# Performance work log

Hardware: AMD Instinct MI355X
Metric: run time of the kernel (lower is better)

The kernel has to match this reference:

```python
import jax, jax.numpy as jnp
import numpy as np
import math

B, T, C, H, L, V = 8, 511, 1024, 16, 8, 128  # T = block_size - 1
D = C // H
FF = 4 * C


def setup_inputs() -> dict:
    key = jax.random.key(0)
    ks = jax.random.split(key, 12)
    std = 0.02
    n = lambda k, s: (jax.random.normal(k, s, dtype=jnp.float32) * std)
    idx = jax.random.randint(ks[0], (B, T), 0, V)
    idx = jnp.where(idx == 2, 3, idx)  # avoid pad token so logits[idx!=2] keeps all rows
    return {
        "idx": idx,
        "tok_emb": n(ks[1], (V, C)),
        "pos_emb": n(ks[2], (T, C)),
        "ln1_w": jnp.ones((L, C)), "ln1_b": jnp.zeros((L, C)),
        "Wq": n(ks[3], (L, C, C)), "bq": jnp.zeros((L, C)),
        "Wk": n(ks[4], (L, C, C)), "bk": jnp.zeros((L, C)),
        "Wv": n(ks[5], (L, C, C)), "bv": jnp.zeros((L, C)),
        "Wp": n(ks[6], (L, C, C)), "bp": jnp.zeros((L, C)),
        "ln2_w": jnp.ones((L, C)), "ln2_b": jnp.zeros((L, C)),
        "W1": n(ks[7], (L, C, FF)), "b1": jnp.zeros((L, FF)),
        "W2": n(ks[8], (L, FF, C)), "b2": jnp.zeros((L, C)),
        "lnf_w": jnp.ones((C,)), "lnf_b": jnp.zeros((C,)),
        "head_w": n(ks[9], (V, C)),
    }


def _ln(x, w, b):
    m = x.mean(-1, keepdims=True)
    v = ((x - m) ** 2).mean(-1, keepdims=True)
    return (x - m) * jax.lax.rsqrt(v + 1e-5) * w + b


def reference(idx, tok_emb, pos_emb, ln1_w, ln1_b, Wq, bq, Wk, bk, Wv, bv, Wp, bp,
              ln2_w, ln2_b, W1, b1, W2, b2, lnf_w, lnf_b, head_w):
    x = tok_emb[idx] + pos_emb[None, :, :]                      # [B,T,C]
    mask = jnp.tril(jnp.ones((T, T), dtype=bool))
    scale = 1.0 / math.sqrt(D)

    def block(x, p):
        h = _ln(x, p["ln1_w"], p["ln1_b"])
        q = (h @ p["Wq"] + p["bq"]).reshape(B, T, H, D).transpose(0, 2, 1, 3)
        k = (h @ p["Wk"] + p["bk"]).reshape(B, T, H, D).transpose(0, 2, 1, 3)
        v = (h @ p["Wv"] + p["bv"]).reshape(B, T, H, D).transpose(0, 2, 1, 3)
        att = jnp.einsum('bhqd,bhkd->bhqk', q, k) * scale       # [B,H,T,T]
        att = jnp.where(mask, att, -jnp.inf)
        att = jax.nn.softmax(att, axis=-1)
        y = jnp.einsum('bhqk,bhkd->bhqd', att, v)
        y = y.transpose(0, 2, 1, 3).reshape(B, T, C)
        x = x + y @ p["Wp"] + p["bp"]
        h = _ln(x, p["ln2_w"], p["ln2_b"])
        h = jax.nn.gelu(h @ p["W1"] + p["b1"], approximate=False)
        x = x + h @ p["W2"] + p["b2"]
        return x, None

    stacked = dict(ln1_w=ln1_w, ln1_b=ln1_b, Wq=Wq, bq=bq, Wk=Wk, bk=bk, Wv=Wv, bv=bv,
                   Wp=Wp, bp=bp, ln2_w=ln2_w, ln2_b=ln2_b, W1=W1, b1=b1, W2=W2, b2=b2)
    x, _ = jax.lax.scan(block, x, stacked)
    x = _ln(x, lnf_w, lnf_b)
    logits = x @ head_w.T                                       # [B,T,V]
    # logits[idx != 2] with no 2-tokens present == all rows flattened
    return logits.reshape(B * T, V)
```

## Files before the change

kernel.cpp:

```cpp
#include <hip/hip_runtime.h>
#include <hip/hip_bf16.h>

typedef unsigned short u16;
typedef unsigned int   u32;
typedef __attribute__((ext_vector_type(8))) __bf16 bf16x8;
typedef __attribute__((ext_vector_type(4))) float  f32x4;

static constexpr int NB  = 8;
static constexpr int TT  = 511;
static constexpr int CC  = 1024;
static constexpr int HH  = 16;
static constexpr int LL  = 8;
static constexpr int VV  = 128;
static constexpr int FF_ = 4096;
static constexpr int MV  = NB * TT;
static constexpr int MP  = 4096;
static constexpr int TP  = 512;

#define DEVI static __device__ __forceinline__

DEVI u16 f2bf(float f) {
  u32 u = __builtin_bit_cast(u32, f);
  u = (u + 0x7fffu + ((u >> 16) & 1u)) >> 16;
  return (u16)u;
}

DEVI void gload16(const void* g, void* lds) {
  auto gp = (const __attribute__((address_space(1))) u32*)(uintptr_t)g;
  auto lp = (__attribute__((address_space(3))) u32*)(uintptr_t)lds;
  __builtin_amdgcn_global_load_lds(gp, lp, 16, 0, 0);
}

__global__ __launch_bounds__(256) void k_transpose(const float* __restrict__ in,
                                                   u16* __restrict__ out, int K, int N,
                                                   size_t is, size_t os) {
  in  += (size_t)blockIdx.z * is;
  out += (size_t)blockIdx.z * os;
  __shared__ u16 tile[64][66];
  int nb = blockIdx.x * 64, kb = blockIdx.y * 64;
  int t = threadIdx.x;
  int r = t >> 4, c4 = (t & 15) * 4;
#pragma unroll
  for (int i = 0; i < 4; ++i) {
    int k = r + i * 16;
    float4 v = *(const float4*)(in + (size_t)(kb + k) * N + nb + c4);
    tile[k][c4 + 0] = f2bf(v.x); tile[k][c4 + 1] = f2bf(v.y);
    tile[k][c4 + 2] = f2bf(v.z); tile[k][c4 + 3] = f2bf(v.w);
  }
  __syncthreads();
#pragma unroll
  for (int i = 0; i < 4; ++i) {
    int n = r + i * 16;
    ushort4 o;
    o.x = tile[c4 + 0][n]; o.y = tile[c4 + 1][n];
    o.z = tile[c4 + 2][n]; o.w = tile[c4 + 3][n];
    *(ushort4*)(out + (size_t)(nb + n) * K + kb + c4) = o;
  }
}

__global__ __launch_bounds__(256) void k_transpose4(const float* __restrict__ Wq,
                                                    const float* __restrict__ Wk,
                                                    const float* __restrict__ Wv,
                                                    const float* __restrict__ Wp,
                                                    u16* __restrict__ wqkv_t,
                                                    u16* __restrict__ wp_t) {
  int z = blockIdx.z, which = z >> 3, lyr = z & 7;
  const float* in; u16* out;
  size_t sq = (size_t)CC * CC;
  if (which == 0)      { in = Wq + lyr * sq; out = wqkv_t + lyr * 3 * sq; }
  else if (which == 1) { in = Wk + lyr * sq; out = wqkv_t + lyr * 3 * sq + sq; }
  else if (which == 2) { in = Wv + lyr * sq; out = wqkv_t + lyr * 3 * sq + 2 * sq; }
  else                 { in = Wp + lyr * sq; out = wp_t + lyr * sq; }
  __shared__ u16 tile[64][66];
  int nb = blockIdx.x * 64, kb = blockIdx.y * 64;
  int t = threadIdx.x;
  int r = t >> 4, c4 = (t & 15) * 4;
#pragma unroll
  for (int i = 0; i < 4; ++i) {
    int k = r + i * 16;
    float4 v = *(const float4*)(in + (size_t)(kb + k) * CC + nb + c4);
    tile[k][c4 + 0] = f2bf(v.x); tile[k][c4 + 1] = f2bf(v.y);
    tile[k][c4 + 2] = f2bf(v.z); tile[k][c4 + 3] = f2bf(v.w);
  }
  __syncthreads();
#pragma unroll
  for (int i = 0; i < 4; ++i) {
    int n = r + i * 16;
    ushort4 o;
    o.x = tile[c4 + 0][n]; o.y = tile[c4 + 1][n];
    o.z = tile[c4 + 2][n]; o.w = tile[c4 + 3][n];
    *(ushort4*)(out + (size_t)(nb + n) * CC + kb + c4) = o;
  }
}

__global__ __launch_bounds__(256) void k_prep(const float* __restrict__ headw,
                                              const float* __restrict__ bq,
                                              const float* __restrict__ bk,
                                              const float* __restrict__ bv,
                                              u16* __restrict__ headb,
                                              float* __restrict__ bqkv) {
  int i = blockIdx.x * 256 + threadIdx.x;
  if (i < VV * CC) {
    headb[i] = f2bf(headw[i]);
  } else {
    int j = i - VV * CC;
    if (j < LL * 3 * CC) {
      int l = j / (3 * CC), c = j % (3 * CC);
      float v = (c < CC) ? bq[l * CC + c] : (c < 2 * CC) ? bk[l * CC + c - CC] : bv[l * CC + c - 2 * CC];
      bqkv[j] = v;
    }
  }
}

__global__ __launch_bounds__(256) void k_embed(const int* __restrict__ idx,
                                               const float* __restrict__ tok,
                                               const float* __restrict__ pos,
                                               float* __restrict__ x) {
  int row = blockIdx.x;
  int c4 = threadIdx.x * 4;
  if (row >= MV) {
    *(float4*)(x + (size_t)row * CC + c4) = make_float4(0.f, 0.f, 0.f, 0.f);
    return;
  }
  int t = row % TT;
  int tid = idx[row];
  float4 a = *(const float4*)(tok + (size_t)tid * CC + c4);
  float4 p = *(const float4*)(pos + (size_t)t * CC + c4);
  a.x += p.x; a.y += p.y; a.z += p.z; a.w += p.w;
  *(float4*)(x + (size_t)row * CC + c4) = a;
}

__global__ __launch_bounds__(256) void k_ln(const float* __restrict__ x,
                                            const float* __restrict__ w,
                                            const float* __restrict__ b,
                                            u16* __restrict__ out) {
  int wid = threadIdx.x >> 6, l = threadIdx.x & 63;
  int row = blockIdx.x * 4 + wid;
  const float* xr = x + (size_t)row * CC;
  float4 v[4];
  float s = 0.f, sq = 0.f;
#pragma unroll
  for (int i = 0; i < 4; ++i) {
    v[i] = *(const float4*)(xr + (i * 64 + l) * 4);
    s  += v[i].x + v[i].y + v[i].z + v[i].w;
    sq += v[i].x * v[i].x + v[i].y * v[i].y + v[i].z * v[i].z + v[i].w * v[i].w;
  }
#pragma unroll
  for (int o = 32; o; o >>= 1) { s += __shfl_xor(s, o); sq += __shfl_xor(sq, o); }
  float mean = s * (1.f / CC);
  float var  = sq * (1.f / CC) - mean * mean;
  float rs = rsqrtf(var + 1e-5f);
#pragma unroll
  for (int i = 0; i < 4; ++i) {
    int c = (i * 64 + l) * 4;
    float4 wv = *(const float4*)(w + c);
    float4 bv = *(const float4*)(b + c);
    ushort4 o4;
    o4.x = f2bf((v[i].x - mean) * rs * wv.x + bv.x);
    o4.y = f2bf((v[i].y - mean) * rs * wv.y + bv.y);
    o4.z = f2bf((v[i].z - mean) * rs * wv.z + bv.z);
    o4.w = f2bf((v[i].w - mean) * rs * wv.w + bv.w);
    *(ushort4*)(out + (size_t)row * CC + c) = o4;
  }
}

template <int EPI>
__global__ __launch_bounds__(512, 1) void k_gemm4(const u16* __restrict__ A,
                                                  const u16* __restrict__ Wt,
                                                  const float* __restrict__ bias,
                                                  u16* __restrict__ outb,
                                                  u16* __restrict__ vt,
                                                  int N, int K, int gridN) {
  __shared__ char lds[2][4][16384];
  int t = threadIdx.x, l = t & 63, wid = t >> 6;
  int wr = wid >> 2, wc = wid & 3;
  int lr = l & 15, lk16 = (l >> 4) * 16;

  int nwg = gridDim.x, wg = blockIdx.x;
  int qq = nwg >> 3, r8 = nwg & 7;
  int xcd = wg & 7, loc = wg >> 3;
  int swz = (xcd < r8 ? xcd * (qq + 1) : r8 * (qq + 1) + (xcd - r8) * qq) + loc;
  int mblk = swz / gridN, nblk = swz - mblk * gridN;
  int mb = mblk * 256, nb = nblk * 256;
  int NT = K >> 6;
  const u16* Ab = A  + (size_t)mb * K;
  const u16* Bb = Wt + (size_t)nb * K;

  int srow = t >> 3, skb = (t & 7) * 16;

  auto stageH = [&](int kt, int ht) {
    int b = kt & 1;
    const u16* src = (ht < 2) ? Ab : Bb;
    int rowbase = (ht & 1) << 7;
    char* dst = &lds[b][ht][0];
    const u16* s0 = src + (size_t)rowbase * K + kt * 64;
#pragma unroll
    for (int j = 0; j < 2; ++j) {
      int row = j * 64 + srow;
      int kb = skb ^ ((row & 7) << 4);
      gload16(s0 + (size_t)row * K + (kb >> 1), dst + j * 8192 + t * 16);
    }
  };

  f32x4 acc[8][4] = {};

  stageH(0, 0); stageH(0, 1); stageH(0, 2); stageH(0, 3);
  stageH(1, 2); stageH(1, 0); stageH(1, 3);
  asm volatile("s_waitcnt vmcnt(6)" ::: "memory");
  __builtin_amdgcn_s_barrier();
  __builtin_amdgcn_sched_barrier(0);

  for (int kt = 0; kt < NT; kt += 2) {
    bool s2 = (kt + 2) < NT, s3 = (kt + 3) < NT;
#pragma unroll
    for (int half = 0; half < 2; ++half) {
      int buf = half;
      bf16x8 Bf[2][4];
#pragma unroll
      for (int q = 0; q < 4; ++q) {
        bf16x8 Af[2][2];
        if (q == 0) {
#pragma unroll
          for (int ks = 0; ks < 2; ++ks)
#pragma unroll
            for (int nf = 0; nf < 4; ++nf) {
              int grow = ((wc & 1) << 6) + nf * 16 + lr;
              int kb = (ks * 64 + lk16) ^ ((grow & 7) << 4);
              Bf[ks][nf] = *(const bf16x8*)(&lds[buf][2 + (wc >> 1)][0] + grow * 128 + kb);
            }
        }
#pragma unroll
        for (int ks = 0; ks < 2; ++ks)
#pragma unroll
          for (int dm = 0; dm < 2; ++dm) {
            int mf = q * 2 + dm;
            int grow = wr * 64 + (mf & 3) * 16 + lr;
            int kb = (ks * 64 + lk16) ^ ((grow & 7) << 4);
            Af[ks][dm] = *(const bf16x8*)(&lds[buf][mf >> 2][0] + grow * 128 + kb);
          }
        if (half == 0) {
          if (q == 0)      stageH(kt + 1, 1);
          else if (q == 1) { if (s2) stageH(kt + 2, 2); }
          else if (q == 2) { if (s2) stageH(kt + 2, 0); }
          else             { if (s2) stageH(kt + 2, 3); }
        } else {
          if (q == 0)      { if (s2) stageH(kt + 2, 1); }
          else if (q == 1) { if (s3) stageH(kt + 3, 2); }
          else if (q == 2) { if (s3) stageH(kt + 3, 0); }
          else             { if (s3) stageH(kt + 3, 3); }
        }
        __builtin_amdgcn_sched_barrier(0);
        __builtin_amdgcn_s_barrier();
        asm volatile("s_waitcnt lgkmcnt(0)" ::: "memory");
        __builtin_amdgcn_sched_barrier(0);
        __builtin_amdgcn_s_setprio(1);
#pragma unroll
        for (int ks = 0; ks < 2; ++ks)
#pragma unroll
          for (int dm = 0; dm < 2; ++dm)
#pragma unroll
            for (int nf = 0; nf < 4; ++nf)
              acc[q * 2 + dm][nf] = __builtin_amdgcn_mfma_f32_16x16x32_bf16(
                  Af[ks][dm], Bf[ks][nf], acc[q * 2 + dm][nf], 0, 0, 0);
        __builtin_amdgcn_s_setprio(0);
        if (q == 3) {
          if (half == 0) {
            if (s2) asm volatile("s_waitcnt vmcnt(6)" ::: "memory");
            else    asm volatile("s_waitcnt vmcnt(0)" ::: "memory");
          } else if (s2) {
            if (s3) asm volatile("s_waitcnt vmcnt(6)" ::: "memory");
            else    asm volatile("s_waitcnt vmcnt(0)" ::: "memory");
          }
        }
        __builtin_amdgcn_sched_barrier(0);
        __builtin_amdgcn_s_barrier();
      }
    }
  }

  int r0 = (l >> 4) * 4;
#pragma unroll
  for (int mf = 0; mf < 8; ++mf) {
    int gr = mb + ((mf >> 2) << 7) + wr * 64 + (mf & 3) * 16 + r0;
#pragma unroll
    for (int nf = 0; nf < 4; ++nf) {
      int gc = nb + wc * 64 + nf * 16 + lr;
      float bv = bias[gc];
      if constexpr (EPI == 1) {
        if (gc >= 2048) {
          int h = (gc - 2048) >> 6, d = gc & 63;
#pragma unroll
          for (int rr = 0; rr < 4; ++rr) {
            int grow = gr + rr;
            if (grow < MV) {
              int b = grow / TT;
              int tt2 = grow - b * TT;
              vt[(((size_t)(b * HH + h)) * 64 + d) * TP + tt2] = f2bf(acc[mf][nf][rr] + bv);
            }
          }
          continue;
        }
      }
#pragma unroll
      for (int rr = 0; rr < 4; ++rr) {
        float v = acc[mf][nf][rr] + bv;
        size_t o = (size_t)(gr + rr) * N + gc;
        if constexpr (EPI == 1) {
          outb[o] = f2bf(v);
        } else {
          float g = 0.5f * v * (1.0f + erff(v * 0.70710678f));
          outb[o] = f2bf(g);
        }
      }
    }
  }
}

template <int EPI>
__global__ __launch_bounds__(256, 2) void k_gemm3(const u16* __restrict__ A,
                                                  const u16* __restrict__ Wt,
                                                  const float* __restrict__ bias,
                                                  float* __restrict__ outf,
                                                  const float* __restrict__ resid,
                                                  int N, int K, int gridN, int Mv) {
  constexpr int BTILE = 16384;
  __shared__ u16 lds[2][128 * 64 * 2];

  int t = threadIdx.x, l = t & 63, wid = t >> 6;
  int wr = wid >> 1, wc = wid & 1;
  int lr = l & 15, lk16 = (l >> 4) * 16;

  int nwg = gridDim.x, wg = blockIdx.x;
  int q = nwg >> 3, r = nwg & 7;
  int xcd = wg & 7, loc = wg >> 3;
  int swz = (xcd < r ? xcd * (q + 1) : r * (q + 1) + (xcd - r) * q) + loc;
  int mblk = swz / gridN;
  int nblk = swz - mblk * gridN;
  int mb = mblk * 128, nb = nblk * 128;
  int NT = K >> 6;
  const u16* Ab = A  + (size_t)mb * K;
  const u16* Bb = Wt + (size_t)nb * K;

  int srow = t >> 3;
  int skb  = (t & 7) * 16;

  auto stage = [&](int kt, int b) {
    const u16* As = Ab + kt * 64;
    char* LD = (char*)&lds[b][0];
#pragma unroll
    for (int j = 0; j < 4; ++j) {
      int row = j * 32 + srow;
      int kb  = skb ^ ((row & 7) << 4);
      gload16(As + (size_t)row * K + (kb >> 1), LD + j * 4096 + t * 16);
    }
    const u16* Bs = Bb + kt * 64;
#pragma unroll
    for (int j = 0; j < 4; ++j) {
      int row = j * 32 + srow;
      int kb  = skb ^ ((row & 7) << 4);
      gload16(Bs + (size_t)row * K + (kb >> 1), LD + BTILE + j * 4096 + t * 16);
    }
  };

  f32x4 acc[4][4] = {};

  auto tile = [&](int b) {
    const char* LA = (const char*)&lds[b][0];
    const char* LB = LA + BTILE;
    bf16x8 bfr[2][4], afr[2][4];
#pragma unroll
    for (int ks = 0; ks < 2; ++ks)
#pragma unroll
      for (int n = 0; n < 4; ++n) {
        int rr = wc * 64 + n * 16 + lr;
        int kb = (ks * 64 + lk16) ^ ((rr & 7) << 4);
        bfr[ks][n] = *(const bf16x8*)(LB + rr * 128 + kb);
      }
#pragma unroll
    for (int ks = 0; ks < 2; ++ks)
#pragma unroll
      for (int m = 0; m < 4; ++m) {
        int rr = wr * 64 + m * 16 + lr;
        int kb = (ks * 64 + lk16) ^ ((rr & 7) << 4);
        afr[ks][m] = *(const bf16x8*)(LA + rr * 128 + kb);
      }
    __builtin_amdgcn_s_setprio(1);
#pragma unroll
    for (int ks = 0; ks < 2; ++ks)
#pragma unroll
      for (int m = 0; m < 4; ++m)
#pragma unroll
        for (int n = 0; n < 4; ++n)
          acc[m][n] = __builtin_amdgcn_mfma_f32_16x16x32_bf16(
              afr[ks][m], bfr[ks][n], acc[m][n], 0, 0, 0);
    __builtin_amdgcn_s_setprio(0);
  };

  stage(0, 0);
  stage(1, 1);
  asm volatile("s_waitcnt vmcnt(8)" ::: "memory");
  __builtin_amdgcn_s_barrier();
  __builtin_amdgcn_sched_barrier(0);

  for (int kt = 0; kt < NT; kt += 2) {
#pragma unroll
    for (int sub = 0; sub < 2; ++sub) {
      tile(sub);
      asm volatile("s_waitcnt lgkmcnt(0)" ::: "memory");
      __builtin_amdgcn_s_barrier();
      __builtin_amdgcn_sched_barrier(0);
      if (kt + 2 + sub < NT) {
        stage(kt + 2 + sub, sub);
        asm volatile("s_waitcnt vmcnt(8)" ::: "memory");
      } else {
        asm volatile("s_waitcnt vmcnt(0)" ::: "memory");
      }
      __builtin_amdgcn_s_barrier();
      __builtin_amdgcn_sched_barrier(0);
    }
  }

  int r0 = (l >> 4) * 4;
#pragma unroll
  for (int m = 0; m < 4; ++m) {
    int gr = mb + wr * 64 + m * 16 + r0;
#pragma unroll
    for (int n = 0; n < 4; ++n) {
      int gc = nb + wc * 64 + n * 16 + lr;
      float bv = 0.f;
      if constexpr (EPI == 0) bv = bias[gc];
#pragma unroll
      for (int rr = 0; rr < 4; ++rr) {
        int grr = gr + rr;
        float v = acc[m][n][rr] + bv;
        size_t o = (size_t)grr * N + gc;
        if constexpr (EPI == 0) {
          outf[o] = v + resid[o];
        } else {
          if (grr < Mv) outf[o] = v;
        }
      }
    }
  }
}

__global__ __launch_bounds__(512, 2) void k_attn2(const u16* __restrict__ qkv,
                                                  const u16* __restrict__ vt,
                                                  u16* __restrict__ y) {
  __shared__ u16 Kb[2][64 * 64];
  __shared__ u16 Vb[2][64 * 64];
  __shared__ u16 Pb[8][16 * 64];
  int t = threadIdx.x, l = t & 63, w = t >> 6;

  int nwg = gridDim.x, wg = blockIdx.x;
  int swz = (wg & 7) * (nwg >> 3) + (wg >> 3);
  int bh = swz >> 2, qt = swz & 3;
  int b = bh >> 4, h = bh & 15;
  int q0 = qt * 128;
  int lr = l & 15, lg = l >> 4, lk8 = lg * 8;

  const float ISC = 0.125f;

  bf16x8 Qa[2];
  {
    int qs = q0 + w * 16 + lr;
    const u16* qp = qkv + (size_t)(b * TT + (qs < TT ? qs : TT - 1)) * 3072 + h * 64;
    Qa[0] = *(const bf16x8*)(qp + lk8);
    Qa[1] = *(const bf16x8*)(qp + 32 + lk8);
  }

  int NT = (q0 + 128) >> 6;

  int srow = w * 8 + (l >> 3);
  int sb16 = (l & 7) * 16;
  int bcol = sb16 ^ ((srow & 7) << 4);
  const u16* Ksrc = qkv + 1024 + h * 64;
  const char* Vsrc = (const char*)(vt + ((size_t)bh * 64 + srow) * TP);

  auto stage = [&](int kt, int buf) {
    int kv0 = kt * 64;
    int kvr = kv0 + srow;
    int krow = b * TT + (kvr < TT ? kvr : TT - 1);
    gload16((const char*)(Ksrc + (size_t)krow * 3072) + bcol, (char*)&Kb[buf][0] + t * 16);
    gload16(Vsrc + kv0 * 2 + bcol, (char*)&Vb[buf][0] + t * 16);
  };

  f32x4 O[4] = {};
  float m_[4], s_[4];
#pragma unroll
  for (int r = 0; r < 4; ++r) { m_[r] = -1e30f; s_[r] = 0.f; }

  stage(0, 0);
  for (int kt = 0; kt < NT; ++kt) {
    int buf = kt & 1;
    if (kt + 1 < NT) {
      stage(kt + 1, buf ^ 1);
      asm volatile("s_waitcnt vmcnt(2)" ::: "memory");
    } else {
      asm volatile("s_waitcnt vmcnt(0)" ::: "memory");
    }
    __builtin_amdgcn_s_barrier();

    int kv0 = kt * 64;
    f32x4 S[4];
    const char* LK = (const char*)&Kb[buf][0];
#pragma unroll
    for (int j = 0; j < 4; ++j) {
      f32x4 a = {};
#pragma unroll
      for (int ks = 0; ks < 2; ++ks) {
        int row = j * 16 + lr;
        int kb = ((ks * 32 + lk8) * 2) ^ ((row & 7) << 4);
        bf16x8 kf = *(const bf16x8*)(LK + row * 128 + kb);
        a = __builtin_amdgcn_mfma_f32_16x16x32_bf16(Qa[ks], kf, a, 0, 0, 0);
      }
      S[j] = a;
    }
    int qbase = q0 + w * 16 + lg * 4;
#pragma unroll
    for (int j = 0; j < 4; ++j) {
      int kv = kv0 + j * 16 + lr;
#pragma unroll
      for (int r = 0; r < 4; ++r) {
        bool valid = (kv <= qbase + r) && (kv < TT);
        S[j][r] = valid ? S[j][r] : -1e30f;
      }
    }
    float mx[4];
#pragma unroll
    for (int r = 0; r < 4; ++r)
      mx[r] = fmaxf(fmaxf(S[0][r], S[1][r]), fmaxf(S[2][r], S[3][r]));
#pragma unroll
    for (int r = 0; r < 4; ++r) {
      mx[r] = fmaxf(mx[r], __shfl_xor(mx[r], 1));
      mx[r] = fmaxf(mx[r], __shfl_xor(mx[r], 2));
      mx[r] = fmaxf(mx[r], __shfl_xor(mx[r], 4));
      mx[r] = fmaxf(mx[r], __shfl_xor(mx[r], 8));
    }
    float sc[4];
#pragma unroll
    for (int r = 0; r < 4; ++r) {
      float mn = fmaxf(m_[r], mx[r]);
      sc[r] = __expf((m_[r] - mn) * ISC);
      m_[r] = mn;
      s_[r] *= sc[r];
    }
#pragma unroll
    for (int j = 0; j < 4; ++j)
#pragma unroll
      for (int r = 0; r < 4; ++r) O[j][r] *= sc[r];
    float rs[4] = {0.f, 0.f, 0.f, 0.f};
    char* LP = (char*)&Pb[w][0];
#pragma unroll
    for (int j = 0; j < 4; ++j) {
#pragma unroll
      for (int r = 0; r < 4; ++r) {
        float p = __expf((S[j][r] - m_[r]) * ISC);
        rs[r] += p;
        int row = lg * 4 + r;
        int addr = (row * 128 + (j * 16 + lr) * 2) ^ ((row & 7) << 4);
        *(u16*)(LP + addr) = f2bf(p);
      }
    }
#pragma unroll
    for (int r = 0; r < 4; ++r) {
      rs[r] += __shfl_xor(rs[r], 1);
      rs[r] += __shfl_xor(rs[r], 2);
      rs[r] += __shfl_xor(rs[r], 4);
      rs[r] += __shfl_xor(rs[r], 8);
      s_[r] += rs[r];
    }
    bf16x8 Pa[2];
#pragma unroll
    for (int ks = 0; ks < 2; ++ks) {
      int addr = (lr * 128 + (ks * 32 + lk8) * 2) ^ ((lr & 7) << 4);
      Pa[ks] = *(const bf16x8*)(LP + addr);
    }
    const char* LV = (const char*)&Vb[buf][0];
#pragma unroll
    for (int j = 0; j < 4; ++j) {
#pragma unroll
      for (int ks = 0; ks < 2; ++ks) {
        int row = j * 16 + lr;
        int kb = ((ks * 32 + lk8) * 2) ^ ((row & 7) << 4);
        bf16x8 vf = *(const bf16x8*)(LV + row * 128 + kb);
        O[j] = __builtin_amdgcn_mfma_f32_16x16x32_bf16(Pa[ks], vf, O[j], 0, 0, 0);
      }
    }
    asm volatile("s_waitcnt lgkmcnt(0)" ::: "memory");
    __builtin_amdgcn_s_barrier();
  }

  int qs0 = q0 + w * 16 + lg * 4;
#pragma unroll
  for (int r = 0; r < 4; ++r) {
    float inv = 1.0f / s_[r];
    int qs = qs0 + r;
    if (qs < TT) {
      u16* yp = y + (size_t)(b * TT + qs) * CC + h * 64;
#pragma unroll
      for (int j = 0; j < 4; ++j)
        yp[j * 16 + lr] = f2bf(O[j][r] * inv);
    }
  }
}

extern "C" void kernel_launch(void* const* d_in, const int* in_sizes, int n_in,
                              void* d_out, int out_size, void* d_ws, size_t ws_size,
                              hipStream_t stream) {
  (void)in_sizes; (void)n_in; (void)out_size; (void)ws_size;
  const int*   idx  = (const int*)  d_in[0];
  const float* tok  = (const float*)d_in[1];
  const float* pos  = (const float*)d_in[2];
  const float* ln1w = (const float*)d_in[3];
  const float* ln1b = (const float*)d_in[4];
  const float* Wq   = (const float*)d_in[5];
  const float* bq   = (const float*)d_in[6];
  const float* Wk   = (const float*)d_in[7];
  const float* bk   = (const float*)d_in[8];
  const float* Wv   = (const float*)d_in[9];
  const float* bv   = (const float*)d_in[10];
  const float* Wp   = (const float*)d_in[11];
  const float* bp   = (const float*)d_in[12];
  const float* ln2w = (const float*)d_in[13];
  const float* ln2b = (const float*)d_in[14];
  const float* W1   = (const float*)d_in[15];
  const float* b1   = (const float*)d_in[16];
  const float* W2   = (const float*)d_in[17];
  const float* b2   = (const float*)d_in[18];
  const float* lnfw = (const float*)d_in[19];
  const float* lnfb = (const float*)d_in[20];
  const float* headw= (const float*)d_in[21];
  float* out = (float*)d_out;

  char* p = (char*)d_ws;
  auto alloc = [&](size_t bytes) { char* r = p; p += (bytes + 255) & ~(size_t)255; return r; };
  u16*   wqkv_t = (u16*)  alloc((size_t)LL * 3 * CC * CC * 2);
  u16*   wp_t   = (u16*)  alloc((size_t)LL * CC * CC * 2);
  u16*   w1_t   = (u16*)  alloc((size_t)LL * FF_ * CC * 2);
  u16*   w2_t   = (u16*)  alloc((size_t)LL * CC * FF_ * 2);
  u16*   headb  = (u16*)  alloc((size_t)VV * CC * 2);
  float* bqkv   = (float*)alloc((size_t)LL * 3 * CC * 4);
  float* x      = (float*)alloc((size_t)MP * CC * 4);
  u16*   hbuf   = (u16*)  alloc((size_t)MP * CC * 2);
  u16*   qkv    = (u16*)  alloc((size_t)MP * 3 * CC * 2);
  u16*   vt     = (u16*)  alloc((size_t)NB * HH * 64 * TP * 2);
  u16*   ybuf   = (u16*)  alloc((size_t)MP * CC * 2);
  u16*   ffb    = (u16*)  alloc((size_t)MP * FF_ * 2);

  k_transpose4<<<dim3(16, 16, 4 * LL), 256, 0, stream>>>(Wq, Wk, Wv, Wp, wqkv_t, wp_t);
  k_transpose<<<dim3(64, 16, LL), 256, 0, stream>>>(W1, w1_t, CC, FF_, (size_t)CC * FF_, (size_t)FF_ * CC);
  k_transpose<<<dim3(16, 64, LL), 256, 0, stream>>>(W2, w2_t, FF_, CC, (size_t)FF_ * CC, (size_t)CC * FF_);
  k_prep<<<(VV * CC + LL * 3 * CC + 255) / 256, 256, 0, stream>>>(headw, bq, bk, bv, headb, bqkv);

  k_embed<<<MP, 256, 0, stream>>>(idx, tok, pos, x);

  for (int l = 0; l < LL; ++l) {
    k_ln<<<MP / 4, 256, 0, stream>>>(x, ln1w + (size_t)l * CC, ln1b + (size_t)l * CC, hbuf);
    k_gemm4<1><<<12 * 16, 512, 0, stream>>>(hbuf, wqkv_t + (size_t)l * 3 * CC * CC,
                                            bqkv + (size_t)l * 3 * CC, qkv, vt, 3 * CC, CC, 12);
    k_attn2<<<NB * HH * 4, 512, 0, stream>>>(qkv, vt, ybuf);
    k_gemm3<0><<<32 * 8, 256, 0, stream>>>(ybuf, wp_t + (size_t)l * CC * CC,
                                           bp + (size_t)l * CC, x, x, CC, CC, 8, MP);
    k_ln<<<MP / 4, 256, 0, stream>>>(x, ln2w + (size_t)l * CC, ln2b + (size_t)l * CC, hbuf);
    k_gemm4<2><<<16 * 16, 512, 0, stream>>>(hbuf, w1_t + (size_t)l * FF_ * CC,
                                            b1 + (size_t)l * FF_, ffb, nullptr, FF_, CC, 16);
    k_gemm3<0><<<32 * 8, 256, 0, stream>>>(ffb, w2_t + (size_t)l * CC * FF_,
                                           b2 + (size_t)l * CC, x, x, CC, FF_, 8, MP);
  }

  k_ln<<<MP / 4, 256, 0, stream>>>(x, lnfw, lnfb, hbuf);
  k_gemm3<3><<<32 * 1, 256, 0, stream>>>(hbuf, headb, nullptr, out, nullptr, VV, CC, 1, MV);
}
```

Baseline: 1.840 ms.

## Split-K the W2 GEMM with fused reduce+residual+LayerNorm, separate V transpose

Replaces the FF down-projection GEMM (K=4096, 128x128 tiles) with a 256x256-tile split-K=4 GEMM writing fp32 partials. A new kernel sums the partials, adds bias and residual, and applies the next layer's LayerNorm (ln1 of the next layer, or the final LN) in the same pass, removing a separate LN launch per layer. It also moves the V-transpose scatter out of the QKV GEMM epilogue into a dedicated LDS-tiled transpose kernel. The cost is 64MB of extra partial-buffer traffic and an added launch, traded for larger tiles, more workgroups and coalesced stores.

```diff
diff --git a/kernel.cpp b/kernel.cpp
--- a/kernel.cpp
+++ b/kernel.cpp
@@ -16,6 +16,7 @@
 static constexpr int MV  = NB * TT;
 static constexpr int MP  = 4096;
 static constexpr int TP  = 512;
+static constexpr size_t PBS = (size_t)MP * CC;
 
 #define DEVI static __device__ __forceinline__
 
@@ -164,12 +165,59 @@
   }
 }
 
+__global__ __launch_bounds__(256) void k_redln(float* __restrict__ x,
+                                               const float* __restrict__ pb,
+                                               const float* __restrict__ bias,
+                                               const float* __restrict__ w,
+                                               const float* __restrict__ b,
+                                               u16* __restrict__ out) {
+  int wid = threadIdx.x >> 6, l = threadIdx.x & 63;
+  int row = blockIdx.x * 4 + wid;
+  float* xr = x + (size_t)row * CC;
+  const float* pr = pb + (size_t)row * CC;
+  float4 v[4];
+  float s = 0.f, sq = 0.f;
+#pragma unroll
+  for (int i = 0; i < 4; ++i) {
+    int c = (i * 64 + l) * 4;
+    float4 xv = *(const float4*)(xr + c);
+    float4 p0 = *(const float4*)(pr + c);
+    float4 p1 = *(const float4*)(pr + PBS + c);
+    float4 p2 = *(const float4*)(pr + 2 * PBS + c);
+    float4 p3 = *(const float4*)(pr + 3 * PBS + c);
+    float4 bb = *(const float4*)(bias + c);
+    v[i].x = xv.x + p0.x + p1.x + p2.x + p3.x + bb.x;
+    v[i].y = xv.y + p0.y + p1.y + p2.y + p3.y + bb.y;
+    v[i].z = xv.z + p0.z + p1.z + p2.z + p3.z + bb.z;
+    v[i].w = xv.w + p0.w + p1.w + p2.w + p3.w + bb.w;
+    *(float4*)(xr + c) = v[i];
+    s  += v[i].x + v[i].y + v[i].z + v[i].w;
+    sq += v[i].x * v[i].x + v[i].y * v[i].y + v[i].z * v[i].z + v[i].w * v[i].w;
+  }
+#pragma unroll
+  for (int o = 32; o; o >>= 1) { s += __shfl_xor(s, o); sq += __shfl_xor(sq, o); }
+  float mean = s * (1.f / CC);
+  float var  = sq * (1.f / CC) - mean * mean;
+  float rs = rsqrtf(var + 1e-5f);
+#pragma unroll
+  for (int i = 0; i < 4; ++i) {
+    int c = (i * 64 + l) * 4;
+    float4 wv = *(const float4*)(w + c);
+    float4 bv = *(const float4*)(b + c);
+    ushort4 o4;
+    o4.x = f2bf((v[i].x - mean) * rs * wv.x + bv.x);
+    o4.y = f2bf((v[i].y - mean) * rs * wv.y + bv.y);
+    o4.z = f2bf((v[i].z - mean) * rs * wv.z + bv.z);
+    o4.w = f2bf((v[i].w - mean) * rs * wv.w + bv.w);
+    *(ushort4*)(out + (size_t)row * CC + c) = o4;
+  }
+}
+
 template <int EPI>
 __global__ __launch_bounds__(512, 1) void k_gemm4(const u16* __restrict__ A,
                                                   const u16* __restrict__ Wt,
                                                   const float* __restrict__ bias,
                                                   u16* __restrict__ outb,
-                                                  u16* __restrict__ vt,
                                                   int N, int K, int gridN) {
   __shared__ char lds[2][4][16384];
   int t = threadIdx.x, l = t & 63, wid = t >> 6;
@@ -286,21 +334,6 @@
     for (int nf = 0; nf < 4; ++nf) {
       int gc = nb + wc * 64 + nf * 16 + lr;
       float bv = bias[gc];
-      if constexpr (EPI == 1) {
-        if (gc >= 2048) {
-          int h = (gc - 2048) >> 6, d = gc & 63;
-#pragma unroll
-          for (int rr = 0; rr < 4; ++rr) {
-            int grow = gr + rr;
-            if (grow < MV) {
-              int b = grow / TT;
-              int tt2 = grow - b * TT;
-              vt[(((size_t)(b * HH + h)) * 64 + d) * TP + tt2] = f2bf(acc[mf][nf][rr] + bv);
-            }
-          }
-          continue;
-        }
-      }
 #pragma unroll
       for (int rr = 0; rr < 4; ++rr) {
         float v = acc[mf][nf][rr] + bv;
@@ -312,6 +345,137 @@
           outb[o] = f2bf(g);
         }
       }
+    }
+  }
+}
+
+__global__ __launch_bounds__(512, 1) void k_gemm4sk(const u16* __restrict__ A,
+                                                    const u16* __restrict__ Wt,
+                                                    float* __restrict__ pbuf,
+                                                    int N, int K, int gridN) {
+  constexpr int KS = 4;
+  __shared__ char lds[2][4][16384];
+  int t = threadIdx.x, l = t & 63, wid = t >> 6;
+  int wr = wid >> 2, wc = wid & 3;
+  int lr = l & 15, lk16 = (l >> 4) * 16;
+
+  int nwg = gridDim.x, wg = blockIdx.x;
+  int qq = nwg >> 3, r8 = nwg & 7;
+  int xcd = wg & 7, loc = wg >> 3;
+  int swz = (xcd < r8 ? xcd * (qq + 1) : r8 * (qq + 1) + (xcd - r8) * qq) + loc;
+  int mblk = swz / (gridN * KS);
+  int rest = swz - mblk * (gridN * KS);
+  int nblk = rest / KS;
+  int kz   = rest - nblk * KS;
+  int mb = mblk * 256, nb = nblk * 256;
+  int Ksub = K / KS;
+  int NT = Ksub >> 6;
+  const u16* Ab = A  + (size_t)mb * K + (size_t)kz * Ksub;
+  const u16* Bb = Wt + (size_t)nb * K + (size_t)kz * Ksub;
+
+  int srow = t >> 3, skb = (t & 7) * 16;
+
+  auto stageH = [&](int kt, int ht) {
+    int b = kt & 1;
+    const u16* src = (ht < 2) ? Ab : Bb;
+    int rowbase = (ht & 1) << 7;
+    char* dst = &lds[b][ht][0];
+    const u16* s0 = src + (size_t)rowbase * K + kt * 64;
+#pragma unroll
+    for (int j = 0; j < 2; ++j) {
+      int row = j * 64 + srow;
+      int kb = skb ^ ((row & 7) << 4);
+      gload16(s0 + (size_t)row * K + (kb >> 1), dst + j * 8192 + t * 16);
+    }
+  };
+
+  f32x4 acc[8][4] = {};
+
+  stageH(0, 0); stageH(0, 1); stageH(0, 2); stageH(0, 3);
+  stageH(1, 2); stageH(1, 0); stageH(1, 3);
+  asm volatile("s_waitcnt vmcnt(6)" ::: "memory");
+  __builtin_amdgcn_s_barrier();
+  __builtin_amdgcn_sched_barrier(0);
+
+  for (int kt = 0; kt < NT; kt += 2) {
+    bool s2 = (kt + 2) < NT, s3 = (kt + 3) < NT;
+#pragma unroll
+    for (int half = 0; half < 2; ++half) {
+      int buf = half;
+      bf16x8 Bf[2][4];
+#pragma unroll
+      for (int q = 0; q < 4; ++q) {
+        bf16x8 Af[2][2];
+        if (q == 0) {
+#pragma unroll
+          for (int ks = 0; ks < 2; ++ks)
+#pragma unroll
+            for (int nf = 0; nf < 4; ++nf) {
+              int grow = ((wc & 1) << 6) + nf * 16 + lr;
+              int kb = (ks * 64 + lk16) ^ ((grow & 7) << 4);
+              Bf[ks][nf] = *(const bf16x8*)(&lds[buf][2 + (wc >> 1)][0] + grow * 128 + kb);
+            }
+        }
+#pragma unroll
+        for (int ks = 0; ks < 2; ++ks)
+#pragma unroll
+          for (int dm = 0; dm < 2; ++dm) {
+            int mf = q * 2 + dm;
+            int grow = wr * 64 + (mf & 3) * 16 + lr;
+            int kb = (ks * 64 + lk16) ^ ((grow & 7) << 4);
+            Af[ks][dm] = *(const bf16x8*)(&lds[buf][mf >> 2][0] + grow * 128 + kb);
+          }
+        if (half == 0) {
+          if (q == 0)      stageH(kt + 1, 1);
+          else if (q == 1) { if (s2) stageH(kt + 2, 2); }
+          else if (q == 2) { if (s2) stageH(kt + 2, 0); }
+          else             { if (s2) stageH(kt + 2, 3); }
+        } else {
+          if (q == 0)      { if (s2) stageH(kt + 2, 1); }
+          else if (q == 1) { if (s3) stageH(kt + 3, 2); }
+          else if (q == 2) { if (s3) stageH(kt + 3, 0); }
+          else             { if (s3) stageH(kt + 3, 3); }
+        }
+        __builtin_amdgcn_sched_barrier(0);
+        __builtin_amdgcn_s_barrier();
+        asm volatile("s_waitcnt lgkmcnt(0)" ::: "memory");
+        __builtin_amdgcn_sched_barrier(0);
+        __builtin_amdgcn_s_setprio(1);
+#pragma unroll
+        for (int ks = 0; ks < 2; ++ks)
+#pragma unroll
+          for (int dm = 0; dm < 2; ++dm)
+#pragma unroll
+            for (int nf = 0; nf < 4; ++nf)
+              acc[q * 2 + dm][nf] = __builtin_amdgcn_mfma_f32_16x16x32_bf16(
+                  Af[ks][dm], Bf[ks][nf], acc[q * 2 + dm][nf], 0, 0, 0);
+        __builtin_amdgcn_s_setprio(0);
+        if (q == 3) {
+          if (half == 0) {
+            if (s2) asm volatile("s_waitcnt vmcnt(6)" ::: "memory");
+            else    asm volatile("s_waitcnt vmcnt(0)" ::: "memory");
+          } else if (s2) {
+            if (s3) asm volatile("s_waitcnt vmcnt(6)" ::: "memory");
+            else    asm volatile("s_waitcnt vmcnt(0)" ::: "memory");
+          }
+        }
+        __builtin_amdgcn_sched_barrier(0);
+        __builtin_amdgcn_s_barrier();
+      }
+    }
+  }
+
+  float* pb = pbuf + (size_t)kz * PBS;
+  int r0 = (l >> 4) * 4;
+#pragma unroll
+  for (int mf = 0; mf < 8; ++mf) {
+    int gr = mb + ((mf >> 2) << 7) + wr * 64 + (mf & 3) * 16 + r0;
+#pragma unroll
+    for (int nf = 0; nf < 4; ++nf) {
+      int gc = nb + wc * 64 + nf * 16 + lr;
+#pragma unroll
+      for (int rr = 0; rr < 4; ++rr)
+        pb[(size_t)(gr + rr) * N + gc] = acc[mf][nf][rr];
     }
   }
 }
@@ -444,6 +608,36 @@
   }
 }
 
+__global__ __launch_bounds__(256) void k_vtrans(const u16* __restrict__ qkv,
+                                                u16* __restrict__ vt) {
+  __shared__ u16 tile[64][66];
+  int bh = blockIdx.y;
+  int b = bh >> 4, h = bh & 15;
+  int t0 = blockIdx.x * 64;
+  int t = threadIdx.x;
+  int r = t >> 4, c4 = (t & 15) * 4;
+#pragma unroll
+  for (int i = 0; i < 4; ++i) {
+    int tt = r + i * 16;
+    int trow = t0 + tt;
+    int srow = b * TT + (trow < TT ? trow : TT - 1);
+    ushort4 v = *(const ushort4*)(qkv + (size_t)srow * 3072 + 2048 + h * 64 + c4);
+    tile[tt][c4 + 0] = v.x; tile[tt][c4 + 1] = v.y;
+    tile[tt][c4 + 2] = v.z; tile[tt][c4 + 3] = v.w;
+  }
+  __syncthreads();
+#pragma unroll
+  for (int i = 0; i < 4; ++i) {
+    int d = r + i * 16;
+    ushort4 o;
+    o.x = (t0 + c4 + 0 < TT) ? tile[c4 + 0][d] : (u16)0;
+    o.y = (t0 + c4 + 1 < TT) ? tile[c4 + 1][d] : (u16)0;
+    o.z = (t0 + c4 + 2 < TT) ? tile[c4 + 2][d] : (u16)0;
+    o.w = (t0 + c4 + 3 < TT) ? tile[c4 + 3][d] : (u16)0;
+    *(ushort4*)(vt + ((size_t)bh * 64 + d) * TP + t0 + c4) = o;
+  }
+}
+
 __global__ __launch_bounds__(512, 2) void k_attn2(const u16* __restrict__ qkv,
                                                   const u16* __restrict__ vt,
                                                   u16* __restrict__ y) {
@@ -608,7 +802,7 @@
 extern "C" void kernel_launch(void* const* d_in, const int* in_sizes, int n_in,
                               void* d_out, int out_size, void* d_ws, size_t ws_size,
                               hipStream_t stream) {
-  (void)in_sizes; (void)n_in; (void)out_size; (void)ws_size;
+  (void)in_sizes; (void)n_in; (void)out_size;
   const int*   idx  = (const int*)  d_in[0];
   const float* tok  = (const float*)d_in[1];
   const float* pos  = (const float*)d_in[2];
@@ -647,6 +841,8 @@
   u16*   vt     = (u16*)  alloc((size_t)NB * HH * 64 * TP * 2);
   u16*   ybuf   = (u16*)  alloc((size_t)MP * CC * 2);
   u16*   ffb    = (u16*)  alloc((size_t)MP * FF_ * 2);
+  float* pbuf   = (float*)alloc((size_t)4 * PBS * 4);
+  bool havePB = ((size_t)(p - (char*)d_ws) <= ws_size);
 
   k_transpose4<<<dim3(16, 16, 4 * LL), 256, 0, stream>>>(Wq, Wk, Wv, Wp, wqkv_t, wp_t);
   k_transpose<<<dim3(64, 16, LL), 256, 0, stream>>>(W1, w1_t, CC, FF_, (size_t)CC * FF_, (size_t)FF_ * CC);
@@ -654,21 +850,29 @@
   k_prep<<<(VV * CC + LL * 3 * CC + 255) / 256, 256, 0, stream>>>(headw, bq, bk, bv, headb, bqkv);
 
   k_embed<<<MP, 256, 0, stream>>>(idx, tok, pos, x);
+  k_ln<<<MP / 4, 256, 0, stream>>>(x, ln1w, ln1b, hbuf);
 
   for (int l = 0; l < LL; ++l) {
-    k_ln<<<MP / 4, 256, 0, stream>>>(x, ln1w + (size_t)l * CC, ln1b + (size_t)l * CC, hbuf);
+    const float* nw = (l < LL - 1) ? ln1w + (size_t)(l + 1) * CC : lnfw;
+    const float* nb = (l < LL - 1) ? ln1b + (size_t)(l + 1) * CC : lnfb;
     k_gemm4<1><<<12 * 16, 512, 0, stream>>>(hbuf, wqkv_t + (size_t)l * 3 * CC * CC,
-                                            bqkv + (size_t)l * 3 * CC, qkv, vt, 3 * CC, CC, 12);
+                                            bqkv + (size_t)l * 3 * CC, qkv, 3 * CC, CC, 12);
+    k_vtrans<<<dim3(8, NB * HH), 256, 0, stream>>>(qkv, vt);
     k_attn2<<<NB * HH * 4, 512, 0, stream>>>(qkv, vt, ybuf);
     k_gemm3<0><<<32 * 8, 256, 0, stream>>>(ybuf, wp_t + (size_t)l * CC * CC,
                                            bp + (size_t)l * CC, x, x, CC, CC, 8, MP);
     k_ln<<<MP / 4, 256, 0, stream>>>(x, ln2w + (size_t)l * CC, ln2b + (size_t)l * CC, hbuf);
     k_gemm4<2><<<16 * 16, 512, 0, stream>>>(hbuf, w1_t + (size_t)l * FF_ * CC,
-                                            b1 + (size_t)l * FF_, ffb, nullptr, FF_, CC, 16);
-    k_gemm3<0><<<32 * 8, 256, 0, stream>>>(ffb, w2_t + (size_t)l * CC * FF_,
-                                           b2 + (size_t)l * CC, x, x, CC, FF_, 8, MP);
-  }
-
-  k_ln<<<MP / 4, 256, 0, stream>>>(x, lnfw, lnfb, hbuf);
+                                            b1 + (size_t)l * FF_, ffb, FF_, CC, 16);
+    if (havePB) {
+      k_gemm4sk<<<16 * 4 * 4, 512, 0, stream>>>(ffb, w2_t + (size_t)l * CC * FF_, pbuf, CC, FF_, 4);
+      k_redln<<<MP / 4, 256, 0, stream>>>(x, pbuf, b2 + (size_t)l * CC, nw, nb, hbuf);
+    } else {
+      k_gemm3<0><<<32 * 8, 256, 0, stream>>>(ffb, w2_t + (size_t)l * CC * FF_,
+                                             b2 + (size_t)l * CC, x, x, CC, FF_, 8, MP);
+      k_ln<<<MP / 4, 256, 0, stream>>>(x, nw, nb, hbuf);
+    }
+  }
+
   k_gemm3<3><<<32 * 1, 256, 0, stream>>>(hbuf, headb, nullptr, out, nullptr, VV, CC, 1, MV);
 }
```

Result: faster. 1.712 ms (-6.9%).
